# Kernel optimization log

Hardware: AMD Instinct MI355X
Metric: run time of the kernel (lower is better)

Reference implementation:

```python
import jax, jax.numpy as jnp
import numpy as np
from jax import lax

WINDOW_SIZE = 11
C1 = 0.01 ** 2
C2 = 0.03 ** 2


def make_window(window_size: int) -> jnp.ndarray:
    # scipy.ndimage.gaussian_filter(np.ones(ws), sigma) with mode='reflect'
    # preserves constant inputs exactly, so gauss_1d == ones(ws).
    # outer(ones, ones) / sum -> uniform box window of weight 1/ws^2.
    return jnp.full((window_size, window_size), 1.0 / (window_size * window_size), dtype=jnp.float32)


def setup_inputs() -> dict:
    key = jax.random.key(0)
    k1, k2 = jax.random.split(key)
    B, C, D, H, W = 1, 1, 64, 512, 512
    x = jax.random.uniform(k1, (B, C, D, H, W), dtype=jnp.float32)
    y = jax.random.uniform(k2, (B, C, D, H, W), dtype=jnp.float32)
    window = make_window(WINDOW_SIZE)
    return {"x": x, "y": y, "window": window}


def _windowed_sum(imgs, window):
    # imgs: [N,1,H,W]; window: [ws,ws]. 'same' cross-correlation (window is symmetric).
    ws = window.shape[0]
    pad = ws // 2
    w = window[None, None, :, :]  # [O=1, I=1, ws, ws]
    return lax.conv_general_dilated(
        imgs, w, window_strides=(1, 1), padding=[(pad, pad), (pad, pad)],
        dimension_numbers=("NCHW", "OIHW", "NCHW"))


def reference(x, y, window):
    B, C, D, H, W = x.shape
    # Fold depth into the conv batch dim: every depth slice is an independent 2D SSIM.
    xs = x.transpose(0, 2, 1, 3, 4).reshape(B * D, C, H, W)
    ys = y.transpose(0, 2, 1, 3, 4).reshape(B * D, C, H, W)
    # Single batched conv over [x, y, x^2, y^2, x*y]
    stacked = jnp.concatenate([xs, ys, xs * xs, ys * ys, xs * ys], axis=0)
    conv = _windowed_sum(stacked, window)
    mu_x, mu_y, e_x2, e_y2, e_xy = jnp.split(conv, 5, axis=0)
    mu_x_sq = mu_x * mu_x
    mu_y_sq = mu_y * mu_y
    mu_xy = mu_x * mu_y
    sigma_x_sq = e_x2 - mu_x_sq
    sigma_y_sq = e_y2 - mu_y_sq
    sigma_xy = e_xy - mu_xy
    ssim_map = ((2.0 * mu_xy + C1) * (2.0 * sigma_xy + C2)) / (
        (mu_x_sq + mu_y_sq + C1) * (sigma_x_sq + sigma_y_sq + C2))
    # Per-slice means averaged over slices == global mean (all slices same size).
    return 1.0 - ssim_map.mean()
```

## Files before the change

kernel.cpp:

```cpp
#include <hip/hip_runtime.h>


constexpr int IMG   = 512;
constexpr int RB    = 8;
constexpr int BANDS = IMG / RB;
constexpr int WPB   = 4;
constexpr int NBLK  = 64 * BANDS / WPB;
constexpr float K1 = 1.4641f;
constexpr float K2 = 13.1769f;

__device__ __forceinline__ float shr1(float v) {
  return __int_as_float(__builtin_amdgcn_update_dpp(
      0, __float_as_int(v), 0x138, 0xF, 0xF, true));
}
__device__ __forceinline__ float shl1(float v) {
  return __int_as_float(__builtin_amdgcn_update_dpp(
      0, __float_as_int(v), 0x130, 0xF, 0xF, true));
}

template <bool ATOMIC>
__global__ __launch_bounds__(256, 2) void ssim_main(const float* __restrict__ x,
                                                    const float* __restrict__ y,
                                                    float* __restrict__ out_ws) {
  __shared__ float wsum[WPB];

  const int tid  = threadIdx.x;
  const int lane = tid & 63;
  const int wid  = tid >> 6;

  const int bid  = blockIdx.x;
  const int xcd  = bid & 7;
  const int qq   = bid >> 3;
  const int z    = xcd * 8 + (qq >> 4);
  const int band = (qq & 15) * WPB + wid;
  const int o0   = band * RB;
  const int gs   = o0 - 5;

  const float* xs = x + (size_t)z * IMG * IMG + lane * 8;
  const float* ys = y + (size_t)z * IMG * IMG + lane * 8;

  float sX[8] = {}, sY[8] = {}, sXX[8] = {}, sYY[8] = {}, sXY[8] = {};
  float cxA[8], cyA[8], oxA[8], oyA[8];
  float cxB[8], cyB[8], oxB[8], oyB[8];
  float acc = 0.f;

  auto ldrow8 = [&](const float* p, bool valid, float (&d)[8]) {
    if (valid) {
      const float4 a = *(const float4*)p;
      const float4 b = *(const float4*)(p + 4);
      d[0] = a.x; d[1] = a.y; d[2] = a.z; d[3] = a.w;
      d[4] = b.x; d[5] = b.y; d[6] = b.z; d[7] = b.w;
    } else {
#pragma unroll
      for (int j = 0; j < 8; ++j) d[j] = 0.f;
    }
  };

  auto hwin = [&](const float (&S)[8], float (&B)[8]) {
    const float vm5  = shr1(S[3]);
    const float vm4  = shr1(S[4]);
    const float vm3  = shr1(S[5]);
    const float vm2  = shr1(S[6]);
    const float vm1  = shr1(S[7]);
    const float vp8  = shl1(S[0]);
    const float vp9  = shl1(S[1]);
    const float vp10 = shl1(S[2]);
    const float vp11 = shl1(S[3]);
    const float vp12 = shl1(S[4]);
    float s = (((vm5 + vm4) + (vm3 + vm2)) + ((vm1 + S[0]) + (S[1] + S[2]))) +
              ((S[3] + S[4]) + S[5]);
    B[0] = s;
    s += S[6]  - vm5;  B[1] = s;
    s += S[7]  - vm4;  B[2] = s;
    s += vp8   - vm3;  B[3] = s;
    s += vp9   - vm2;  B[4] = s;
    s += vp10  - vm1;  B[5] = s;
    s += vp11  - S[0]; B[6] = s;
    s += vp12  - S[1]; B[7] = s;
  };

  auto step = [&](int i, bool steady,
                  float (&cx)[8], float (&cy)[8], float (&ox)[8], float (&oy)[8],
                  float (&nx)[8], float (&ny)[8], float (&px)[8], float (&py)[8]) {
    const int gr = gs + i;
    const bool nv = ((unsigned)(gr + 1) < (unsigned)IMG) && (i < RB + 9);
    ldrow8(xs + (gr + 1) * IMG, nv, nx);
    ldrow8(ys + (gr + 1) * IMG, nv, ny);

    if (steady) {
      const int gro = gr - 10;
      const bool ov = (gro >= 0) && (i < RB + 9);
      ldrow8(xs + gro * IMG, ov, px);
      ldrow8(ys + gro * IMG, ov, py);
#pragma unroll
      for (int j = 0; j < 8; ++j) {
        sX[j] += cx[j] - ox[j];
        sY[j] += cy[j] - oy[j];
        sXX[j] = fmaf(cx[j], cx[j], fmaf(-ox[j], ox[j], sXX[j]));
        sYY[j] = fmaf(cy[j], cy[j], fmaf(-oy[j], oy[j], sYY[j]));
        sXY[j] = fmaf(cx[j], cy[j], fmaf(-ox[j], oy[j], sXY[j]));
      }
      float bX[8], bY[8], bXX[8], bYY[8], bXY[8];
      hwin(sX, bX); hwin(sY, bY); hwin(sXX, bXX); hwin(sYY, bYY); hwin(sXY, bXY);
#pragma unroll
      for (int j2 = 0; j2 < 8; ++j2) {
        const float bx  = bX[j2];
        const float by  = bY[j2];
        const float bxy = bx * by;
        const float sq  = fmaf(bx, bx, by * by);
        const float n1  = fmaf(2.f, bxy, K1);
        const float n2  = fmaf(242.f, bXY[j2], fmaf(-2.f, bxy, K2));
        const float d1  = sq + K1;
        const float d2  = fmaf(121.f, bXX[j2] + bYY[j2], K2 - sq);
        acc += (n1 * n2) * __builtin_amdgcn_rcpf(d1 * d2);
      }
    } else {
#pragma unroll
      for (int j = 0; j < 8; ++j) {
        sX[j] += cx[j];
        sY[j] += cy[j];
        sXX[j] = fmaf(cx[j], cx[j], sXX[j]);
        sYY[j] = fmaf(cy[j], cy[j], sYY[j]);
        sXY[j] = fmaf(cx[j], cy[j], sXY[j]);
      }
    }
  };

  ldrow8(xs + gs * IMG, gs >= 0, cxA);
  ldrow8(ys + gs * IMG, gs >= 0, cyA);
#pragma unroll
  for (int j = 0; j < 8; ++j) {
    oxA[j] = 0.f; oyA[j] = 0.f; oxB[j] = 0.f; oyB[j] = 0.f;
  }

#pragma unroll 1
  for (int i = 0; i < 10; i += 2) {
    step(i,     false, cxA, cyA, oxA, oyA, cxB, cyB, oxB, oyB);
    step(i + 1, false, cxB, cyB, oxB, oyB, cxA, cyA, oxA, oyA);
  }
#pragma unroll 1
  for (int i = 10; i < RB + 10; i += 2) {
    step(i,     true, cxA, cyA, oxA, oyA, cxB, cyB, oxB, oyB);
    step(i + 1, true, cxB, cyB, oxB, oyB, cxA, cyA, oxA, oyA);
  }

#pragma unroll
  for (int off = 32; off > 0; off >>= 1) acc += __shfl_down(acc, off, 64);
  if (lane == 0) wsum[wid] = acc;
  __syncthreads();
  if (tid == 0) {
    const float t = wsum[0] + wsum[1] + wsum[2] + wsum[3];
    if (ATOMIC) {
      atomicAdd(out_ws, t);
    } else {
      out_ws[bid] = t;
    }
  }
}

__global__ void ssim_finalize(const float* __restrict__ partials, int n,
                              float* __restrict__ out) {
  __shared__ float wsum[4];
  float acc = 0.f;
  for (int i = threadIdx.x; i < n; i += 256) acc += partials[i];
#pragma unroll
  for (int off = 32; off > 0; off >>= 1) acc += __shfl_down(acc, off, 64);
  if ((threadIdx.x & 63) == 0) wsum[threadIdx.x >> 6] = acc;
  __syncthreads();
  if (threadIdx.x == 0) {
    const float t = wsum[0] + wsum[1] + wsum[2] + wsum[3];
    out[0] = 1.0f - t * (1.0f / (64.0f * 512.0f * 512.0f));
  }
}

__global__ void ssim_zero(float* p) {
  if (threadIdx.x == 0) p[0] = 0.f;
}

__global__ void ssim_finalize_atomic(const float* __restrict__ accp,
                                     float* __restrict__ out) {
  if (threadIdx.x == 0)
    out[0] = 1.0f - accp[0] * (1.0f / (64.0f * 512.0f * 512.0f));
}

extern "C" void kernel_launch(void* const* d_in, const int* in_sizes, int n_in,
                              void* d_out, int out_size, void* d_ws, size_t ws_size,
                              hipStream_t stream) {
  const float* x = (const float*)d_in[0];
  const float* y = (const float*)d_in[1];
  float* out = (float*)d_out;

  dim3 grid(NBLK);
  dim3 block(256);

  if (ws_size >= (size_t)NBLK * sizeof(float)) {
    float* partials = (float*)d_ws;
    ssim_main<false><<<grid, block, 0, stream>>>(x, y, partials);
    ssim_finalize<<<1, 256, 0, stream>>>(partials, NBLK, out);
  } else {
    float* accp = (float*)d_ws;
    ssim_zero<<<1, 64, 0, stream>>>(accp);
    ssim_main<true><<<grid, block, 0, stream>>>(x, y, accp);
    ssim_finalize_atomic<<<1, 64, 0, stream>>>(accp, out);
  }
}
```

Before: 179.3 us.

## Keep first seven rows in a register ring instead of reloading outgoing rows

Fully unrolls the vertical sliding window and holds the first seven loaded rows of x and y in a register ring. The rows leaving the window are read from registers rather than fetched from global memory a second time. This cuts global loads per band from roughly 34 rows to 18, at the cost of about 112 extra live registers, which may cause spills or lower occupancy under launch_bounds(256,2).

```diff
diff --git a/kernel.cpp b/kernel.cpp
--- a/kernel.cpp
+++ b/kernel.cpp
@@ -40,8 +40,8 @@
   const float* ys = y + (size_t)z * IMG * IMG + lane * 8;
 
   float sX[8] = {}, sY[8] = {}, sXX[8] = {}, sYY[8] = {}, sXY[8] = {};
-  float cxA[8], cyA[8], oxA[8], oyA[8];
-  float cxB[8], cyB[8], oxB[8], oyB[8];
+  float ringx[7][8], ringy[7][8];
+  float t0x[8], t0y[8], t1x[8], t1y[8];
   float acc = 0.f;
 
   auto ldrow8 = [&](const float* p, bool valid, float (&d)[8]) {
@@ -53,6 +53,36 @@
     } else {
 #pragma unroll
       for (int j = 0; j < 8; ++j) d[j] = 0.f;
+    }
+  };
+
+  auto LD = [&](int i, float (&dx)[8], float (&dy)[8]) {
+    const int gr = gs + i;
+    const bool v = (unsigned)gr < (unsigned)IMG;
+    ldrow8(xs + (size_t)gr * IMG, v, dx);
+    ldrow8(ys + (size_t)gr * IMG, v, dy);
+  };
+
+  auto accum = [&](const float (&cx)[8], const float (&cy)[8]) {
+#pragma unroll
+    for (int j = 0; j < 8; ++j) {
+      sX[j] += cx[j];
+      sY[j] += cy[j];
+      sXX[j] = fmaf(cx[j], cx[j], sXX[j]);
+      sYY[j] = fmaf(cy[j], cy[j], sYY[j]);
+      sXY[j] = fmaf(cx[j], cy[j], sXY[j]);
+    }
+  };
+
+  auto stepv = [&](const float (&cx)[8], const float (&cy)[8],
+                   const float (&ox)[8], const float (&oy)[8]) {
+#pragma unroll
+    for (int j = 0; j < 8; ++j) {
+      sX[j] += cx[j] - ox[j];
+      sY[j] += cy[j] - oy[j];
+      sXX[j] = fmaf(cx[j], cx[j], fmaf(-ox[j], ox[j], sXX[j]));
+      sYY[j] = fmaf(cy[j], cy[j], fmaf(-oy[j], oy[j], sYY[j]));
+      sXY[j] = fmaf(cx[j], cy[j], fmaf(-ox[j], oy[j], sXY[j]));
     }
   };
 
@@ -79,70 +109,60 @@
     s += vp12  - S[1]; B[7] = s;
   };
 
-  auto step = [&](int i, bool steady,
-                  float (&cx)[8], float (&cy)[8], float (&ox)[8], float (&oy)[8],
-                  float (&nx)[8], float (&ny)[8], float (&px)[8], float (&py)[8]) {
-    const int gr = gs + i;
-    const bool nv = ((unsigned)(gr + 1) < (unsigned)IMG) && (i < RB + 9);
-    ldrow8(xs + (gr + 1) * IMG, nv, nx);
-    ldrow8(ys + (gr + 1) * IMG, nv, ny);
-
-    if (steady) {
-      const int gro = gr - 10;
-      const bool ov = (gro >= 0) && (i < RB + 9);
-      ldrow8(xs + gro * IMG, ov, px);
-      ldrow8(ys + gro * IMG, ov, py);
-#pragma unroll
-      for (int j = 0; j < 8; ++j) {
-        sX[j] += cx[j] - ox[j];
-        sY[j] += cy[j] - oy[j];
-        sXX[j] = fmaf(cx[j], cx[j], fmaf(-ox[j], ox[j], sXX[j]));
-        sYY[j] = fmaf(cy[j], cy[j], fmaf(-oy[j], oy[j], sYY[j]));
-        sXY[j] = fmaf(cx[j], cy[j], fmaf(-ox[j], oy[j], sXY[j]));
-      }
-      float bX[8], bY[8], bXX[8], bYY[8], bXY[8];
-      hwin(sX, bX); hwin(sY, bY); hwin(sXX, bXX); hwin(sYY, bYY); hwin(sXY, bXY);
-#pragma unroll
-      for (int j2 = 0; j2 < 8; ++j2) {
-        const float bx  = bX[j2];
-        const float by  = bY[j2];
-        const float bxy = bx * by;
-        const float sq  = fmaf(bx, bx, by * by);
-        const float n1  = fmaf(2.f, bxy, K1);
-        const float n2  = fmaf(242.f, bXY[j2], fmaf(-2.f, bxy, K2));
-        const float d1  = sq + K1;
-        const float d2  = fmaf(121.f, bXX[j2] + bYY[j2], K2 - sq);
-        acc += (n1 * n2) * __builtin_amdgcn_rcpf(d1 * d2);
-      }
-    } else {
-#pragma unroll
-      for (int j = 0; j < 8; ++j) {
-        sX[j] += cx[j];
-        sY[j] += cy[j];
-        sXX[j] = fmaf(cx[j], cx[j], sXX[j]);
-        sYY[j] = fmaf(cy[j], cy[j], sYY[j]);
-        sXY[j] = fmaf(cx[j], cy[j], sXY[j]);
-      }
-    }
-  };
-
-  ldrow8(xs + gs * IMG, gs >= 0, cxA);
-  ldrow8(ys + gs * IMG, gs >= 0, cyA);
-#pragma unroll
-  for (int j = 0; j < 8; ++j) {
-    oxA[j] = 0.f; oyA[j] = 0.f; oxB[j] = 0.f; oyB[j] = 0.f;
-  }
-
-#pragma unroll 1
-  for (int i = 0; i < 10; i += 2) {
-    step(i,     false, cxA, cyA, oxA, oyA, cxB, cyB, oxB, oyB);
-    step(i + 1, false, cxB, cyB, oxB, oyB, cxA, cyA, oxA, oyA);
-  }
-#pragma unroll 1
-  for (int i = 10; i < RB + 10; i += 2) {
-    step(i,     true, cxA, cyA, oxA, oyA, cxB, cyB, oxB, oyB);
-    step(i + 1, true, cxB, cyB, oxB, oyB, cxA, cyA, oxA, oyA);
-  }
+  auto outp = [&]() {
+    float bX[8], bY[8], bXX[8], bYY[8], bXY[8];
+    hwin(sX, bX); hwin(sY, bY); hwin(sXX, bXX); hwin(sYY, bYY); hwin(sXY, bXY);
+#pragma unroll
+    for (int j = 0; j < 8; ++j) {
+      const float bx  = bX[j];
+      const float by  = bY[j];
+      const float bxy = bx * by;
+      const float sq  = fmaf(bx, bx, by * by);
+      const float n1  = fmaf(2.f, bxy, K1);
+      const float n2  = fmaf(242.f, bXY[j], fmaf(-2.f, bxy, K2));
+      const float d1  = sq + K1;
+      const float d2  = fmaf(121.f, bXX[j] + bYY[j], K2 - sq);
+      acc += (n1 * n2) * __builtin_amdgcn_rcpf(d1 * d2);
+    }
+  };
+
+  LD(0, ringx[0], ringy[0]);
+  LD(1, ringx[1], ringy[1]);
+  accum(ringx[0], ringy[0]);
+  LD(2, ringx[2], ringy[2]);
+  accum(ringx[1], ringy[1]);
+  LD(3, ringx[3], ringy[3]);
+  accum(ringx[2], ringy[2]);
+  LD(4, ringx[4], ringy[4]);
+  accum(ringx[3], ringy[3]);
+  LD(5, ringx[5], ringy[5]);
+  accum(ringx[4], ringy[4]);
+  LD(6, ringx[6], ringy[6]);
+  accum(ringx[5], ringy[5]);
+  LD(7, t0x, t0y);
+  accum(ringx[6], ringy[6]);
+  LD(8, t1x, t1y);
+  accum(t0x, t0y);
+  LD(9, t0x, t0y);
+  accum(t1x, t1y);
+  LD(10, t1x, t1y);
+  accum(t0x, t0y);
+  LD(11, t0x, t0y);
+  accum(t1x, t1y);
+  outp();
+  LD(12, t1x, t1y);
+  stepv(t0x, t0y, ringx[0], ringy[0]); outp();
+  LD(13, t0x, t0y);
+  stepv(t1x, t1y, ringx[1], ringy[1]); outp();
+  LD(14, t1x, t1y);
+  stepv(t0x, t0y, ringx[2], ringy[2]); outp();
+  LD(15, t0x, t0y);
+  stepv(t1x, t1y, ringx[3], ringy[3]); outp();
+  LD(16, t1x, t1y);
+  stepv(t0x, t0y, ringx[4], ringy[4]); outp();
+  LD(17, t0x, t0y);
+  stepv(t1x, t1y, ringx[5], ringy[5]); outp();
+  stepv(t0x, t0y, ringx[6], ringy[6]); outp();
 
 #pragma unroll
   for (int off = 32; off > 0; off >>= 1) acc += __shfl_down(acc, off, 64);
```

Result: slower. 390.5 us (+117.8%).

## Double rows per band and software-pipeline branchless row loads

Applied to the files above, without the earlier changes.

Each wave now computes 16 output rows instead of 8. This lowers the share of work spent on the 10-row halo and the warm-up accumulation, and it halves the grid. Row loads become branchless: the row index is clamped and out-of-image rows are zeroed by a multiplicative mask. Sched barriers place the next row's loads before the current row's consume and output math so memory latency overlaps compute. The trade-off is fewer resident waves per CU for latency hiding, plus a few extra multiplies for masking.

```diff
diff --git a/kernel.cpp b/kernel.cpp
--- a/kernel.cpp
+++ b/kernel.cpp
@@ -2,7 +2,7 @@
 
 
 constexpr int IMG   = 512;
-constexpr int RB    = 8;
+constexpr int RB    = 16;
 constexpr int BANDS = IMG / RB;
 constexpr int WPB   = 4;
 constexpr int NBLK  = 64 * BANDS / WPB;
@@ -31,8 +31,8 @@
   const int bid  = blockIdx.x;
   const int xcd  = bid & 7;
   const int qq   = bid >> 3;
-  const int z    = xcd * 8 + (qq >> 4);
-  const int band = (qq & 15) * WPB + wid;
+  const int z    = xcd * 8 + (qq >> 3);
+  const int band = (qq & 7) * WPB + wid;
   const int o0   = band * RB;
   const int gs   = o0 - 5;
 
@@ -42,17 +42,47 @@
   float sX[8] = {}, sY[8] = {}, sXX[8] = {}, sYY[8] = {}, sXY[8] = {};
   float cxA[8], cyA[8], oxA[8], oyA[8];
   float cxB[8], cyB[8], oxB[8], oyB[8];
+  float mcA = 0.f, mcB = 0.f, moA = 1.f, moB = 1.f;
   float acc = 0.f;
 
-  auto ldrow8 = [&](const float* p, bool valid, float (&d)[8]) {
-    if (valid) {
-      const float4 a = *(const float4*)p;
-      const float4 b = *(const float4*)(p + 4);
-      d[0] = a.x; d[1] = a.y; d[2] = a.z; d[3] = a.w;
-      d[4] = b.x; d[5] = b.y; d[6] = b.z; d[7] = b.w;
-    } else {
-#pragma unroll
-      for (int j = 0; j < 8; ++j) d[j] = 0.f;
+  auto LDraw = [&](int gr, float (&dx)[8], float (&dy)[8]) -> float {
+    const int grc = gr < 0 ? 0 : (gr > IMG - 1 ? IMG - 1 : gr);
+    const float* px = xs + (size_t)grc * IMG;
+    const float* py = ys + (size_t)grc * IMG;
+    const float4 a = *(const float4*)px;
+    const float4 b = *(const float4*)(px + 4);
+    const float4 c = *(const float4*)py;
+    const float4 d = *(const float4*)(py + 4);
+    dx[0] = a.x; dx[1] = a.y; dx[2] = a.z; dx[3] = a.w;
+    dx[4] = b.x; dx[5] = b.y; dx[6] = b.z; dx[7] = b.w;
+    dy[0] = c.x; dy[1] = c.y; dy[2] = c.z; dy[3] = c.w;
+    dy[4] = d.x; dy[5] = d.y; dy[6] = d.z; dy[7] = d.w;
+    return ((unsigned)gr < (unsigned)IMG) ? 1.f : 0.f;
+  };
+
+  auto consumeW = [&](const float (&cx)[8], const float (&cy)[8], float mc) {
+#pragma unroll
+    for (int j = 0; j < 8; ++j) {
+      const float cxm = cx[j] * mc, cym = cy[j] * mc;
+      sX[j] += cxm;
+      sY[j] += cym;
+      sXX[j] = fmaf(cx[j], cxm, sXX[j]);
+      sYY[j] = fmaf(cy[j], cym, sYY[j]);
+      sXY[j] = fmaf(cx[j], cym, sXY[j]);
+    }
+  };
+
+  auto consumeS = [&](const float (&cx)[8], const float (&cy)[8], float mc,
+                      const float (&ox)[8], const float (&oy)[8], float mo) {
+#pragma unroll
+    for (int j = 0; j < 8; ++j) {
+      const float cxm = cx[j] * mc, cym = cy[j] * mc;
+      const float oxm = ox[j] * mo, oym = oy[j] * mo;
+      sX[j] += cxm - oxm;
+      sY[j] += cym - oym;
+      sXX[j] = fmaf(cx[j], cxm, fmaf(-ox[j], oxm, sXX[j]));
+      sYY[j] = fmaf(cy[j], cym, fmaf(-oy[j], oym, sYY[j]));
+      sXY[j] = fmaf(cx[j], cym, fmaf(-ox[j], oym, sXY[j]));
     }
   };
 
@@ -79,55 +109,24 @@
     s += vp12  - S[1]; B[7] = s;
   };
 
-  auto step = [&](int i, bool steady,
-                  float (&cx)[8], float (&cy)[8], float (&ox)[8], float (&oy)[8],
-                  float (&nx)[8], float (&ny)[8], float (&px)[8], float (&py)[8]) {
-    const int gr = gs + i;
-    const bool nv = ((unsigned)(gr + 1) < (unsigned)IMG) && (i < RB + 9);
-    ldrow8(xs + (gr + 1) * IMG, nv, nx);
-    ldrow8(ys + (gr + 1) * IMG, nv, ny);
-
-    if (steady) {
-      const int gro = gr - 10;
-      const bool ov = (gro >= 0) && (i < RB + 9);
-      ldrow8(xs + gro * IMG, ov, px);
-      ldrow8(ys + gro * IMG, ov, py);
-#pragma unroll
-      for (int j = 0; j < 8; ++j) {
-        sX[j] += cx[j] - ox[j];
-        sY[j] += cy[j] - oy[j];
-        sXX[j] = fmaf(cx[j], cx[j], fmaf(-ox[j], ox[j], sXX[j]));
-        sYY[j] = fmaf(cy[j], cy[j], fmaf(-oy[j], oy[j], sYY[j]));
-        sXY[j] = fmaf(cx[j], cy[j], fmaf(-ox[j], oy[j], sXY[j]));
-      }
-      float bX[8], bY[8], bXX[8], bYY[8], bXY[8];
-      hwin(sX, bX); hwin(sY, bY); hwin(sXX, bXX); hwin(sYY, bYY); hwin(sXY, bXY);
-#pragma unroll
-      for (int j2 = 0; j2 < 8; ++j2) {
-        const float bx  = bX[j2];
-        const float by  = bY[j2];
-        const float bxy = bx * by;
-        const float sq  = fmaf(bx, bx, by * by);
-        const float n1  = fmaf(2.f, bxy, K1);
-        const float n2  = fmaf(242.f, bXY[j2], fmaf(-2.f, bxy, K2));
-        const float d1  = sq + K1;
-        const float d2  = fmaf(121.f, bXX[j2] + bYY[j2], K2 - sq);
-        acc += (n1 * n2) * __builtin_amdgcn_rcpf(d1 * d2);
-      }
-    } else {
-#pragma unroll
-      for (int j = 0; j < 8; ++j) {
-        sX[j] += cx[j];
-        sY[j] += cy[j];
-        sXX[j] = fmaf(cx[j], cx[j], sXX[j]);
-        sYY[j] = fmaf(cy[j], cy[j], sYY[j]);
-        sXY[j] = fmaf(cx[j], cy[j], sXY[j]);
-      }
-    }
-  };
-
-  ldrow8(xs + gs * IMG, gs >= 0, cxA);
-  ldrow8(ys + gs * IMG, gs >= 0, cyA);
+  auto outp = [&]() {
+    float bX[8], bY[8], bXX[8], bYY[8], bXY[8];
+    hwin(sX, bX); hwin(sY, bY); hwin(sXX, bXX); hwin(sYY, bYY); hwin(sXY, bXY);
+#pragma unroll
+    for (int j = 0; j < 8; ++j) {
+      const float bx  = bX[j];
+      const float by  = bY[j];
+      const float bxy = bx * by;
+      const float sq  = fmaf(bx, bx, by * by);
+      const float n1  = fmaf(2.f, bxy, K1);
+      const float n2  = fmaf(242.f, bXY[j], fmaf(-2.f, bxy, K2));
+      const float d1  = sq + K1;
+      const float d2  = fmaf(121.f, bXX[j] + bYY[j], K2 - sq);
+      acc += (n1 * n2) * __builtin_amdgcn_rcpf(d1 * d2);
+    }
+  };
+
+  mcA = LDraw(gs, cxA, cyA);
 #pragma unroll
   for (int j = 0; j < 8; ++j) {
     oxA[j] = 0.f; oyA[j] = 0.f; oxB[j] = 0.f; oyB[j] = 0.f;
@@ -135,13 +134,26 @@
 
 #pragma unroll 1
   for (int i = 0; i < 10; i += 2) {
-    step(i,     false, cxA, cyA, oxA, oyA, cxB, cyB, oxB, oyB);
-    step(i + 1, false, cxB, cyB, oxB, oyB, cxA, cyA, oxA, oyA);
-  }
+    mcB = LDraw(gs + i + 1, cxB, cyB);
+    __builtin_amdgcn_sched_barrier(0);
+    consumeW(cxA, cyA, mcA);
+    mcA = LDraw(gs + i + 2, cxA, cyA);
+    __builtin_amdgcn_sched_barrier(0);
+    consumeW(cxB, cyB, mcB);
+  }
+
 #pragma unroll 1
   for (int i = 10; i < RB + 10; i += 2) {
-    step(i,     true, cxA, cyA, oxA, oyA, cxB, cyB, oxB, oyB);
-    step(i + 1, true, cxB, cyB, oxB, oyB, cxA, cyA, oxA, oyA);
+    mcB = LDraw(gs + i + 1, cxB, cyB);
+    moB = LDraw(gs + i - 10, oxB, oyB);
+    __builtin_amdgcn_sched_barrier(0);
+    consumeS(cxA, cyA, mcA, oxA, oyA, moA);
+    outp();
+    mcA = LDraw(gs + i + 2, cxA, cyA);
+    moA = LDraw(gs + i - 9, oxA, oyA);
+    __builtin_amdgcn_sched_barrier(0);
+    consumeS(cxB, cyB, mcB, oxB, oyB, moB);
+    outp();
   }
 
 #pragma unroll
```

After: 172.0 us. -4.0%, faster.
